# Kernel tuning notes

Measured on AMD Instinct MI355X. Metric: run time of the kernel, lower is better.

Reference implementation:

```python
import jax, jax.numpy as jnp
import numpy as np

POI, EMB, UNITS, QDIM, B = 5000, 256, 512, 256, 64


def setup_inputs() -> dict:
    key = jax.random.key(0)
    ks = jax.random.split(key, 16)
    s = 0.05
    return {
        "x": jax.random.randint(ks[0], (B,), 0, POI),
        "query": jax.random.normal(ks[1], (B, QDIM), jnp.float32),
        "poi_embedding": jax.random.normal(ks[2], (POI, EMB), jnp.float32),
        "A_hat": jax.random.normal(ks[3], (B, B), jnp.float32),
        "dec_hidden": jax.random.normal(ks[4], (B, UNITS), jnp.float32),
        "cat_dec_hidden": jax.random.normal(ks[5], (1, B, UNITS), jnp.float32),
        # GRUCell params (keras order z, r, h; reset_after=True -> bias [2, 3*units])
        "gru_kernel": jax.random.normal(ks[6], (EMB + QDIM, 3 * UNITS), jnp.float32) * s,
        "gru_rec_kernel": jax.random.normal(ks[7], (UNITS, 3 * UNITS), jnp.float32) * s,
        "gru_bias": jax.random.normal(ks[8], (2, 3 * UNITS), jnp.float32) * s,
        # Bahdanau attention params
        "W1_w": jax.random.normal(ks[9], (EMB, UNITS), jnp.float32) * s,
        "W1_b": jnp.zeros((UNITS,), jnp.float32),
        "W2_w": jax.random.normal(ks[10], (UNITS, UNITS), jnp.float32) * s,
        "W2_b": jnp.zeros((UNITS,), jnp.float32),
        "V_w": jax.random.normal(ks[11], (UNITS, 1), jnp.float32) * s,
        "V_b": jnp.zeros((1,), jnp.float32),
        # output dense: concat(context EMB, output_ UNITS, cat_hidden UNITS) -> POI
        "fc_w": jax.random.normal(ks[12], (EMB + 2 * UNITS, POI), jnp.float32) * s,
        "fc_b": jnp.zeros((POI,), jnp.float32),
    }


def _gru_cell(x, h, kernel, rec_kernel, bias):
    # keras GRUCell, reset_after=True, gate order (z, r, h)
    xm = x @ kernel + bias[0]        # [B, 3U]
    hm = h @ rec_kernel + bias[1]    # [B, 3U]
    xz, xr, xh = jnp.split(xm, 3, axis=-1)
    hz, hr, hh = jnp.split(hm, 3, axis=-1)
    z = jax.nn.sigmoid(xz + hz)
    r = jax.nn.sigmoid(xr + hr)
    h_cand = jnp.tanh(xh + r * hh)
    h_new = z * h + (1.0 - z) * h_cand
    return h_new, h_new


def reference(x, query, poi_embedding, A_hat, dec_hidden, cat_dec_hidden,
              gru_kernel, gru_rec_kernel, gru_bias,
              W1_w, W1_b, W2_w, W2_b, V_w, V_b, fc_w, fc_b):
    emb = poi_embedding
    x1 = jnp.concatenate([emb[x], query], axis=1)          # [B, EMB+QDIM]
    output_, state = _gru_cell(x1, dec_hidden, gru_kernel, gru_rec_kernel, gru_bias)
    # Bahdanau attention: values are the full embedding table [POI, EMB]
    v_proj = emb @ W1_w + W1_b                              # [POI, U]
    q_proj = output_ @ W2_w + W2_b                          # [B, U]
    score = jnp.tanh(v_proj[None, :, :] + q_proj[:, None, :]) @ V_w + V_b  # [B, POI, 1]
    attn = jax.nn.softmax(score, axis=1)                    # [B, POI, 1]
    context = jnp.sum(attn * emb[None, :, :], axis=1)       # [B, EMB]
    out_cat = jnp.concatenate([context, output_, cat_dec_hidden[0]], axis=1)
    logits = out_cat @ fc_w + fc_b                          # [B, POI]
    return (logits, state, output_)
```

## Files before the change

kernel.cpp:

```cpp
#include <hip/hip_runtime.h>
#include <hip/hip_bf16.h>

typedef __bf16 bf16;
typedef __bf16 bf16x8 __attribute__((ext_vector_type(8)));
typedef float f32x4 __attribute__((ext_vector_type(4)));

#define BB 64
#define EMB 256
#define UNITS 512
#define POI 5000
#define KCAT 1280
#define SCLD 5024
#define L2E 1.4426950408889634f

__device__ __forceinline__ float rcp_(float x){ return __builtin_amdgcn_rcpf(x); }
__device__ __forceinline__ float exp2_(float x){ return __builtin_amdgcn_exp2f(x); }

__device__ __forceinline__ f32x4 mm16r(const float* __restrict__ ap, const float* __restrict__ B,
                                       int ldb, int K, int nc, int lane){
  int q = lane >> 4;
  f32x4 acc = {0.f,0.f,0.f,0.f};
  ap += q*8;
  const float* bp = B + (size_t)(q*8)*ldb + nc;
#pragma unroll 2
  for(int k0 = 0; k0 < K; k0 += 32){
    f32x4 a0 = *(const f32x4*)ap;
    f32x4 a1 = *(const f32x4*)(ap+4);
    bf16x8 a, b;
#pragma unroll
    for(int j=0;j<4;j++){ a[j] = (bf16)a0[j]; a[4+j] = (bf16)a1[j]; }
#pragma unroll
    for(int j=0;j<8;j++) b[j] = (bf16)bp[(size_t)j*ldb];
    acc = __builtin_amdgcn_mfma_f32_16x16x32_bf16(a, b, acc, 0, 0, 0);
    ap += 32; bp += (size_t)32*ldb;
  }
  return acc;
}

__device__ __forceinline__ f32x4 mm16f(const float* __restrict__ A, const float* __restrict__ B,
                                       int lda, int ldb, int K, int mr, int nc, int lane){
  return mm16r(A + (size_t)mr*lda, B, ldb, K, nc, lane);
}

__global__ __launch_bounds__(256) void k_gru(const int* __restrict__ x, const float* __restrict__ query,
    const float* __restrict__ emb, const float* __restrict__ h0,
    const float* __restrict__ gruK, const float* __restrict__ gruR,
    float* __restrict__ xmP, float* __restrict__ hmP){
  int lane = threadIdx.x & 63, w = threadIdx.x >> 6;
  int col = blockIdx.x*16 + (lane & 15);
  int z = blockIdx.z;
  int mr = w*16 + (lane & 15);
  const float* arow;
  const float* B;
  float* C;
  if(blockIdx.y){
    arow = h0 + (size_t)mr*512 + z*256;
    B = gruR + (size_t)(z*256)*1536;
    C = hmP + (size_t)z*BB*1536;
  } else {
    arow = z ? (query + (size_t)mr*256) : (emb + (size_t)x[mr]*EMB);
    B = gruK + (size_t)(z*256)*1536;
    C = xmP + (size_t)z*BB*1536;
  }
  f32x4 acc = mm16r(arow, B, 1536, 256, col, lane);
  int rb = w*16 + (lane >> 4)*4;
#pragma unroll
  for(int r=0;r<4;r++) C[(size_t)(rb+r)*1536 + col] = acc[r];
}

__global__ void k_gates(const float* __restrict__ xmP, const float* __restrict__ hmP,
                        const float* __restrict__ bias, const float* __restrict__ h0,
                        const float* __restrict__ catd,
                        float* __restrict__ hn, float* __restrict__ outc, float* __restrict__ dout){
  int b = blockIdx.x, u = threadIdx.x;
  const float* x0 = xmP + b*1536; const float* x1s = xmP + (size_t)BB*1536 + b*1536;
  const float* h0s = hmP + b*1536; const float* h1s = hmP + (size_t)BB*1536 + b*1536;
  float xz = x0[u]      + x1s[u]      + bias[u];
  float xg = x0[512+u]  + x1s[512+u]  + bias[512+u];
  float xh = x0[1024+u] + x1s[1024+u] + bias[1024+u];
  float hz = h0s[u]      + h1s[u]      + bias[1536+u];
  float hg = h0s[512+u]  + h1s[512+u]  + bias[2048+u];
  float hh = h0s[1024+u] + h1s[1024+u] + bias[2560+u];
  float z = rcp_(1.f + exp2_(-L2E*(xz+hz)));
  float r = rcp_(1.f + exp2_(-L2E*(xg+hg)));
  float ca = xh + r*hh;
  ca = fminf(fmaxf(ca, -15.f), 15.f);
  float e = exp2_(2.f*L2E*ca);
  float hc = (e - 1.f)*rcp_(e + 1.f);
  float h = h0[b*512+u];
  float v = z*h + (1.f - z)*hc;
  hn[b*512+u] = v;
  outc[b*KCAT + 256 + u] = v;
  outc[b*KCAT + 768 + u] = catd[(size_t)b*512 + u];
  dout[(size_t)POI*BB + (size_t)b*512 + u] = v;
  dout[(size_t)POI*BB + (size_t)BB*512 + (size_t)b*512 + u] = v;
}

__global__ __launch_bounds__(256) void k_qproj(const float* __restrict__ hn, const float* __restrict__ W2,
                        const float* __restrict__ W2b, float* __restrict__ Eq){
  int lane = threadIdx.x & 63, w = threadIdx.x >> 6;
  int col = blockIdx.x*16 + (lane & 15);
  f32x4 acc = mm16f(hn, W2, UNITS, UNITS, UNITS, w*16 + (lane & 15), col, lane);
  float bn = W2b[col];
  int rb = w*16 + (lane >> 4)*4;
#pragma unroll
  for(int r=0;r<4;r++){
    float v = (acc[r] + bn)*(2.f*L2E);
    Eq[(rb+r)*UNITS + col] = exp2_(fminf(fmaxf(v, -40.f), 40.f));
  }
}

template<int NY>
__global__ __launch_bounds__(256, 6) void k_vscore(const float* __restrict__ emb, const float* __restrict__ W1,
    const float* __restrict__ W1b, const float* __restrict__ Eq,
    const float* __restrict__ Vw, float* __restrict__ scS){
  constexpr int USL = 512/NY;
  __shared__ float evs[16][USL+4];
  __shared__ float vws[USL];
  int t = threadIdx.x, lane = t & 63, w = t >> 6;
  int p0 = blockIdx.x*16, uh = blockIdx.y*USL;
  int mr = p0 + (lane & 15); if(mr > POI-1) mr = POI-1;
#pragma unroll
  for(int i=0;i<USL/64;i++){
    int ncl = (w + i*4)*16 + (lane & 15);
    f32x4 acc = mm16f(emb, W1, EMB, UNITS, EMB, mr, uh + ncl, lane);
    float bn = W1b[uh + ncl];
    int rb = (lane >> 4)*4;
#pragma unroll
    for(int r=0;r<4;r++){
      float v = (acc[r] + bn)*(2.f*L2E);
      evs[rb+r][ncl] = exp2_(fminf(fmaxf(v, -40.f), 40.f));
    }
  }
  if(t < USL) vws[t] = Vw[uh + t];
  __syncthreads();
  int tp = t & 7, tb = t >> 3;
  const float* q0p = Eq + (size_t)(2*tb)*UNITS + uh;
  const float* q1p = q0p + UNITS;
  float s00=0.f, s01=0.f, s10=0.f, s11=0.f;
#pragma unroll 2
  for(int u4=0; u4<USL/4; ++u4){
    f32x4 e0 = *(const f32x4*)&evs[2*tp][4*u4];
    f32x4 e1 = *(const f32x4*)&evs[2*tp+1][4*u4];
    f32x4 q0 = *(const f32x4*)&q0p[4*u4];
    f32x4 q1 = *(const f32x4*)&q1p[4*u4];
    f32x4 w4 = *(const f32x4*)&vws[4*u4];
#pragma unroll
    for(int e=0;e<4;e++){
      float wv = w4[e];
      s00 += wv * rcp_(e0[e]*q0[e] + 1.f);
      s01 += wv * rcp_(e0[e]*q1[e] + 1.f);
      s10 += wv * rcp_(e1[e]*q0[e] + 1.f);
      s11 += wv * rcp_(e1[e]*q1[e] + 1.f);
    }
  }
  float* s = scS + (size_t)blockIdx.y*BB*SCLD;
  int pA = p0 + 2*tp, bA = 2*tb;
  if(pA < POI)  { s[(size_t)bA*SCLD + pA]   = s00; s[(size_t)(bA+1)*SCLD + pA]   = s01; }
  if(pA+1 < POI){ s[(size_t)bA*SCLD + pA+1] = s10; s[(size_t)(bA+1)*SCLD + pA+1] = s11; }
}

__global__ __launch_bounds__(512) void k_softmax(float* __restrict__ sc, const float* __restrict__ Vw,
                                                 float* __restrict__ outc, int nslab){
  __shared__ float red[512];
  int b = blockIdx.x, t = threadIdx.x;
  if(t < 256) outc[b*KCAT + t] = 0.f;
  red[t] = Vw[t];
  __syncthreads();
  for(int o=256;o>0;o>>=1){ if(t<o) red[t]+=red[t+o]; __syncthreads(); }
  float SW = red[0]; __syncthreads();
  float* sA = sc + (size_t)b*SCLD;
  float mx = -3.4e38f;
  for(int p=t;p<POI;p+=512){
    float acc = sA[p];
    for(int y=1;y<nslab;y++) acc += sA[(size_t)y*BB*SCLD + p];
    float s = SW - 2.f*acc;
    sA[p] = s;
    mx = fmaxf(mx, s);
  }
  red[t] = mx; __syncthreads();
  for(int o=256;o>0;o>>=1){ if(t<o) red[t]=fmaxf(red[t],red[t+o]); __syncthreads(); }
  float M = red[0]; __syncthreads();
  float sum = 0.f;
  for(int p=t;p<POI;p+=512){
    float wv = exp2_((sA[p] - M)*L2E);
    sA[p] = wv;
    sum += wv;
  }
  red[t] = sum; __syncthreads();
  for(int o=256;o>0;o>>=1){ if(t<o) red[t]+=red[t+o]; __syncthreads(); }
  float iv = rcp_(red[0]);
  for(int p=t;p<POI;p+=512) sA[p] *= iv;
  if(t < SCLD-POI) sA[POI + t] = 0.f;
}

__global__ __launch_bounds__(256) void k_ctx(const float* __restrict__ wb, const float* __restrict__ emb,
                                             float* __restrict__ outc){
  int lane = threadIdx.x & 63, w = threadIdx.x >> 6;
  int n = blockIdx.x*16 + (lane & 15);
  int ky = blockIdx.y;
  int kbeg = ky*384;
  int mr = w*16 + (lane & 15);
  f32x4 acc = mm16f(wb + kbeg, emb + (size_t)kbeg*EMB, SCLD, EMB, 384, mr, n, lane);
  if(ky == 12){
    int q = lane >> 4;
    const float* ap = wb + (size_t)mr*SCLD + 4992 + q*8;
    bf16x8 a, bfr;
#pragma unroll
    for(int j=0;j<8;j++) a[j] = (bf16)ap[j];
#pragma unroll
    for(int j=0;j<8;j++){
      int k = 4992 + q*8 + j; int kc = k < POI ? k : POI-1;
      bfr[j] = (bf16)emb[(size_t)kc*EMB + n];
    }
    acc = __builtin_amdgcn_mfma_f32_16x16x32_bf16(a, bfr, acc, 0, 0, 0);
  }
  int rb = w*16 + (lane >> 4)*4;
#pragma unroll
  for(int r=0;r<4;r++) atomicAdd(&outc[(size_t)(rb+r)*KCAT + n], acc[r]);
}

__global__ __launch_bounds__(256) void k_logits(const float* __restrict__ A, const float* __restrict__ Bw,
                        const float* __restrict__ fcb, float* __restrict__ out){
  int lane = threadIdx.x & 63, w = threadIdx.x >> 6;
  int n = blockIdx.x*16 + (lane & 15);
  int nc = n < POI ? n : POI-1;
  int ky = blockIdx.y, kbeg = ky*320;
  f32x4 acc = mm16f(A + kbeg, Bw + (size_t)kbeg*POI, KCAT, POI, 320,
                    w*16 + (lane & 15), nc, lane);
  int rb = w*16 + (lane >> 4)*4;
  if(n < POI){
    float bn = (ky == 0) ? fcb[n] : 0.f;
#pragma unroll
    for(int r=0;r<4;r++) atomicAdd(&out[(size_t)(rb+r)*POI + n], acc[r] + bn);
  }
}

extern "C" void kernel_launch(void* const* d_in, const int* in_sizes, int n_in,
                              void* d_out, int out_size, void* d_ws, size_t ws_size,
                              hipStream_t stream){
  const int*   x     = (const int*)d_in[0];
  const float* query = (const float*)d_in[1];
  const float* emb   = (const float*)d_in[2];
  const float* h0    = (const float*)d_in[4];
  const float* catd  = (const float*)d_in[5];
  const float* gruK  = (const float*)d_in[6];
  const float* gruR  = (const float*)d_in[7];
  const float* gruB  = (const float*)d_in[8];
  const float* W1    = (const float*)d_in[9];
  const float* W1b   = (const float*)d_in[10];
  const float* W2    = (const float*)d_in[11];
  const float* W2b   = (const float*)d_in[12];
  const float* Vw    = (const float*)d_in[13];
  const float* fcw   = (const float*)d_in[15];
  const float* fcb   = (const float*)d_in[16];
  float* out = (float*)d_out;

  int nslab = (ws_size >= (size_t)14*1024*1024) ? 8 : 4;

  char* ws = (char*)d_ws;
  size_t off = 0;
  auto alloc = [&](size_t bytes)->void*{ void* p = ws + off; off += (bytes + 255) & ~(size_t)255; return p; };
  float* outc = (float*)alloc((size_t)BB*KCAT*4);
  float* xmP  = (float*)alloc((size_t)2*BB*1536*4);
  float* hmP  = (float*)alloc((size_t)2*BB*1536*4);
  float* hn   = (float*)alloc((size_t)BB*512*4);
  float* Eq   = (float*)alloc((size_t)BB*512*4);
  float* sc   = (float*)alloc((size_t)nslab*BB*SCLD*4);

  hipMemsetAsync(out, 0, (size_t)BB*POI*sizeof(float), stream);
  k_gru    <<<dim3(96,2,2), 256, 0, stream>>>(x, query, emb, h0, gruK, gruR, xmP, hmP);
  k_gates  <<<BB, 512, 0, stream>>>(xmP, hmP, gruB, h0, catd, hn, outc, out);
  k_qproj  <<<32, 256, 0, stream>>>(hn, W2, W2b, Eq);
  if(nslab == 8)
    k_vscore<8><<<dim3(313,8), 256, 0, stream>>>(emb, W1, W1b, Eq, Vw, sc);
  else
    k_vscore<4><<<dim3(313,4), 256, 0, stream>>>(emb, W1, W1b, Eq, Vw, sc);
  k_softmax<<<BB, 512, 0, stream>>>(sc, Vw, outc, nslab);
  k_ctx    <<<dim3(16,13), 256, 0, stream>>>(sc, emb, outc);
  k_logits <<<dim3(313,4), 256, 0, stream>>>(outc, fcw, fcb, out);
}
```

Before: 207.5 us.

## Retile attention score kernel with transposed W1, LDS query staging, deferred softmax normalization

Adds a prep kernel that zeroes the output and transposes W1, so the vscore MFMA B-operand loads become contiguous vector loads instead of strided scalar loads. Each vscore block now covers 32 POIs instead of 16, stages Eq in shared memory, stores exp values transposed and writes scores as float4. The softmax no longer rescales the score buffer; the reciprocal sum is instead applied in the context kernel's atomic adds. The costs are more shared memory per block with lower occupancy (launch bounds 4), an extra small kernel, and a higher workspace threshold for the 8-slab path.

```diff
diff --git a/kernel.cpp b/kernel.cpp
--- a/kernel.cpp
+++ b/kernel.cpp
@@ -40,6 +40,16 @@
 __device__ __forceinline__ f32x4 mm16f(const float* __restrict__ A, const float* __restrict__ B,
                                        int lda, int ldb, int K, int mr, int nc, int lane){
   return mm16r(A + (size_t)mr*lda, B, ldb, K, nc, lane);
+}
+
+__global__ __launch_bounds__(256) void k_prep0(const float* __restrict__ W1,
+    float* __restrict__ W1T, float* __restrict__ out){
+  int t = blockIdx.x*256 + threadIdx.x;
+  for(int i=t; i<BB*POI; i+=32768) out[i] = 0.f;
+  for(int i=t; i<EMB*UNITS; i+=32768){
+    int r = i >> 9, c = i & 511;
+    W1T[(size_t)c*EMB + r] = W1[i];
+  }
 }
 
 __global__ __launch_bounds__(256) void k_gru(const int* __restrict__ x, const float* __restrict__ query,
@@ -111,57 +121,88 @@
 }
 
 template<int NY>
-__global__ __launch_bounds__(256, 6) void k_vscore(const float* __restrict__ emb, const float* __restrict__ W1,
+__global__ __launch_bounds__(256, 4) void k_vscore(
+    const float* __restrict__ emb, const float* __restrict__ W1T,
     const float* __restrict__ W1b, const float* __restrict__ Eq,
     const float* __restrict__ Vw, float* __restrict__ scS){
   constexpr int USL = 512/NY;
-  __shared__ float evs[16][USL+4];
+  __shared__ float evsT[USL][36];
+  __shared__ float qs[64][USL+4];
   __shared__ float vws[USL];
   int t = threadIdx.x, lane = t & 63, w = t >> 6;
-  int p0 = blockIdx.x*16, uh = blockIdx.y*USL;
-  int mr = p0 + (lane & 15); if(mr > POI-1) mr = POI-1;
+  int p0 = blockIdx.x*32, uh = blockIdx.y*USL;
+  int q = lane >> 4;
 #pragma unroll
   for(int i=0;i<USL/64;i++){
-    int ncl = (w + i*4)*16 + (lane & 15);
-    f32x4 acc = mm16f(emb, W1, EMB, UNITS, EMB, mr, uh + ncl, lane);
-    float bn = W1b[uh + ncl];
-    int rb = (lane >> 4)*4;
-#pragma unroll
-    for(int r=0;r<4;r++){
-      float v = (acc[r] + bn)*(2.f*L2E);
-      evs[rb+r][ncl] = exp2_(fminf(fmaxf(v, -40.f), 40.f));
+    int colL = (w + 4*i)*16 + (lane & 15);
+    float bn = W1b[uh + colL];
+    const float* brow = W1T + (size_t)(uh+colL)*EMB + q*8;
+#pragma unroll
+    for(int pq=0;pq<2;pq++){
+      int mr = p0 + pq*16 + (lane & 15); if(mr >= POI) mr = POI-1;
+      const float* ap = emb + (size_t)mr*EMB + q*8;
+      const float* bp = brow;
+      f32x4 acc = {0.f,0.f,0.f,0.f};
+#pragma unroll 2
+      for(int k0=0;k0<EMB;k0+=32){
+        f32x4 a0 = *(const f32x4*)ap, a1 = *(const f32x4*)(ap+4);
+        f32x4 b0 = *(const f32x4*)bp, b1 = *(const f32x4*)(bp+4);
+        bf16x8 a, b;
+#pragma unroll
+        for(int j=0;j<4;j++){ a[j]=(bf16)a0[j]; a[4+j]=(bf16)a1[j];
+                              b[j]=(bf16)b0[j]; b[4+j]=(bf16)b1[j]; }
+        acc = __builtin_amdgcn_mfma_f32_16x16x32_bf16(a,b,acc,0,0,0);
+        ap += 32; bp += 32;
+      }
+      f32x4 ev;
+#pragma unroll
+      for(int r=0;r<4;r++){
+        float v = (acc[r] + bn)*(2.f*L2E);
+        ev[r] = exp2_(fminf(fmaxf(v,-40.f),40.f));
+      }
+      *(f32x4*)&evsT[colL][pq*16 + q*4] = ev;
     }
+  }
+  constexpr int CG = USL/4;
+  for(int i=t; i<64*CG; i+=256){
+    int b = i/CG, cg = i - b*CG;
+    *(f32x4*)&qs[b][cg*4] = *(const f32x4*)&Eq[b*UNITS + uh + cg*4];
   }
   if(t < USL) vws[t] = Vw[uh + t];
   __syncthreads();
-  int tp = t & 7, tb = t >> 3;
-  const float* q0p = Eq + (size_t)(2*tb)*UNITS + uh;
-  const float* q1p = q0p + UNITS;
-  float s00=0.f, s01=0.f, s10=0.f, s11=0.f;
+  int pg = t & 7, bg = t >> 3;
+  const float* q0r = &qs[2*bg][0];
+  const float* q1r = &qs[2*bg+1][0];
+  f32x4 s0 = {0.f,0.f,0.f,0.f}, s1 = {0.f,0.f,0.f,0.f};
 #pragma unroll 2
   for(int u4=0; u4<USL/4; ++u4){
-    f32x4 e0 = *(const f32x4*)&evs[2*tp][4*u4];
-    f32x4 e1 = *(const f32x4*)&evs[2*tp+1][4*u4];
-    f32x4 q0 = *(const f32x4*)&q0p[4*u4];
-    f32x4 q1 = *(const f32x4*)&q1p[4*u4];
-    f32x4 w4 = *(const f32x4*)&vws[4*u4];
-#pragma unroll
-    for(int e=0;e<4;e++){
-      float wv = w4[e];
-      s00 += wv * rcp_(e0[e]*q0[e] + 1.f);
-      s01 += wv * rcp_(e0[e]*q1[e] + 1.f);
-      s10 += wv * rcp_(e1[e]*q0[e] + 1.f);
-      s11 += wv * rcp_(e1[e]*q1[e] + 1.f);
+    f32x4 q0 = *(const f32x4*)&q0r[u4*4];
+    f32x4 q1 = *(const f32x4*)&q1r[u4*4];
+    f32x4 wv = *(const f32x4*)&vws[u4*4];
+#pragma unroll
+    for(int j=0;j<4;j++){
+      f32x4 ev = *(const f32x4*)&evsT[u4*4+j][4*pg];
+#pragma unroll
+      for(int e=0;e<4;e++){
+        s0[e] += wv[j]*rcp_(ev[e]*q0[j] + 1.f);
+        s1[e] += wv[j]*rcp_(ev[e]*q1[j] + 1.f);
+      }
     }
   }
-  float* s = scS + (size_t)blockIdx.y*BB*SCLD;
-  int pA = p0 + 2*tp, bA = 2*tb;
-  if(pA < POI)  { s[(size_t)bA*SCLD + pA]   = s00; s[(size_t)(bA+1)*SCLD + pA]   = s01; }
-  if(pA+1 < POI){ s[(size_t)bA*SCLD + pA+1] = s10; s[(size_t)(bA+1)*SCLD + pA+1] = s11; }
+  float* srow = scS + (size_t)blockIdx.y*BB*SCLD + (size_t)(2*bg)*SCLD + p0 + 4*pg;
+  int pA = p0 + 4*pg;
+  if(pA + 3 < POI){
+    *(f32x4*)srow = s0;
+    *(f32x4*)(srow + SCLD) = s1;
+  } else {
+#pragma unroll
+    for(int e=0;e<4;e++) if(pA+e < POI){ srow[e] = s0[e]; srow[SCLD+e] = s1[e]; }
+  }
 }
 
 __global__ __launch_bounds__(512) void k_softmax(float* __restrict__ sc, const float* __restrict__ Vw,
-                                                 float* __restrict__ outc, int nslab){
+                                                 float* __restrict__ outc, float* __restrict__ ivb,
+                                                 int nslab){
   __shared__ float red[512];
   int b = blockIdx.x, t = threadIdx.x;
   if(t < 256) outc[b*KCAT + t] = 0.f;
@@ -189,13 +230,12 @@
   }
   red[t] = sum; __syncthreads();
   for(int o=256;o>0;o>>=1){ if(t<o) red[t]+=red[t+o]; __syncthreads(); }
-  float iv = rcp_(red[0]);
-  for(int p=t;p<POI;p+=512) sA[p] *= iv;
+  if(t == 0) ivb[b] = rcp_(red[0]);
   if(t < SCLD-POI) sA[POI + t] = 0.f;
 }
 
 __global__ __launch_bounds__(256) void k_ctx(const float* __restrict__ wb, const float* __restrict__ emb,
-                                             float* __restrict__ outc){
+                                             const float* __restrict__ ivb, float* __restrict__ outc){
   int lane = threadIdx.x & 63, w = threadIdx.x >> 6;
   int n = blockIdx.x*16 + (lane & 15);
   int ky = blockIdx.y;
@@ -217,7 +257,7 @@
   }
   int rb = w*16 + (lane >> 4)*4;
 #pragma unroll
-  for(int r=0;r<4;r++) atomicAdd(&outc[(size_t)(rb+r)*KCAT + n], acc[r]);
+  for(int r=0;r<4;r++) atomicAdd(&outc[(size_t)(rb+r)*KCAT + n], acc[r]*ivb[rb+r]);
 }
 
 __global__ __launch_bounds__(256) void k_logits(const float* __restrict__ A, const float* __restrict__ Bw,
@@ -256,7 +296,7 @@
   const float* fcb   = (const float*)d_in[16];
   float* out = (float*)d_out;
 
-  int nslab = (ws_size >= (size_t)14*1024*1024) ? 8 : 4;
+  int nslab = (ws_size >= (size_t)16*1024*1024) ? 8 : 4;
 
   char* ws = (char*)d_ws;
   size_t off = 0;
@@ -266,17 +306,19 @@
   float* hmP  = (float*)alloc((size_t)2*BB*1536*4);
   float* hn   = (float*)alloc((size_t)BB*512*4);
   float* Eq   = (float*)alloc((size_t)BB*512*4);
+  float* W1T  = (float*)alloc((size_t)UNITS*EMB*4);
+  float* ivb  = (float*)alloc((size_t)BB*4);
   float* sc   = (float*)alloc((size_t)nslab*BB*SCLD*4);
 
-  hipMemsetAsync(out, 0, (size_t)BB*POI*sizeof(float), stream);
+  k_prep0  <<<128, 256, 0, stream>>>(W1, W1T, out);
   k_gru    <<<dim3(96,2,2), 256, 0, stream>>>(x, query, emb, h0, gruK, gruR, xmP, hmP);
   k_gates  <<<BB, 512, 0, stream>>>(xmP, hmP, gruB, h0, catd, hn, outc, out);
   k_qproj  <<<32, 256, 0, stream>>>(hn, W2, W2b, Eq);
   if(nslab == 8)
-    k_vscore<8><<<dim3(313,8), 256, 0, stream>>>(emb, W1, W1b, Eq, Vw, sc);
+    k_vscore<8><<<dim3(157,8), 256, 0, stream>>>(emb, W1T, W1b, Eq, Vw, sc);
   else
-    k_vscore<4><<<dim3(313,4), 256, 0, stream>>>(emb, W1, W1b, Eq, Vw, sc);
-  k_softmax<<<BB, 512, 0, stream>>>(sc, Vw, outc, nslab);
-  k_ctx    <<<dim3(16,13), 256, 0, stream>>>(sc, emb, outc);
+    k_vscore<4><<<dim3(157,4), 256, 0, stream>>>(emb, W1T, W1b, Eq, Vw, sc);
+  k_softmax<<<BB, 512, 0, stream>>>(sc, Vw, outc, ivb, nslab);
+  k_ctx    <<<dim3(16,13), 256, 0, stream>>>(sc, emb, ivb, outc);
   k_logits <<<dim3(313,4), 256, 0, stream>>>(outc, fcw, fcb, out);
 }
```

Result: slower. 218.6 us (+5.4%).
